# Performance work log

Measured on AMD Instinct MI355X. Metric: run time of the kernel, lower is better.

Reference implementation:

```python
import jax, jax.numpy as jnp
import numpy as np


def setup_inputs() -> dict:
    key = jax.random.key(0)
    k1, k2 = jax.random.split(key)
    out = jax.random.uniform(k1, (32, 128, 128, 9, 5), dtype=jnp.float32)
    target = jax.random.uniform(k2, (32, 128, 128, 3, 6), dtype=jnp.float32)
    return {"out": out, "target": target}


def _loss(out, target):
    # out: [B, GX, GY, A, 5], target: [B, GX, GY, Q, 6]
    B, GX, GY, Q, _ = target.shape
    A = out.shape[3]
    # the original loop breaks after qub == 0, so only the first gt per cell is used
    st = target[:, :, :, 0, :]            # [B, GX, GY, 6]
    pos = st[..., 5] > 0.8                # [B, GX, GY] positive-cell mask

    dtype = out.dtype
    # grid-cell centers zxdwx / zxdwy
    zx = (jnp.arange(GX, dtype=dtype) / GX + 1.0 / (2 * GX))[None, :, None, None]
    zy = (jnp.arange(GY, dtype=dtype) / GY + 1.0 / (2 * GY))[None, None, :, None]

    # gt box (center format) -> corners; broadcast over anchor dim
    acx = st[..., 0][..., None]
    acy = st[..., 1][..., None]
    aw = st[..., 2][..., None]
    ah = st[..., 3][..., None]
    ax1, ay1, ax2, ay2 = acx - aw / 2, acy - ah / 2, acx + aw / 2, acy + ah / 2

    # predicted box: offsets decoded relative to grid cell
    bcx = out[..., 0] - 0.5 + zx
    bcy = out[..., 1] - 0.5 + zy
    bw = out[..., 2] - 0.5 + 1.0 / GX
    bh = out[..., 3] - 0.5 + 1.0 / GY
    bx1, by1, bx2, by2 = bcx - bw / 2, bcy - bh / 2, bcx + bw / 2, bcy + bh / 2

    # IoU (intersection zeroed when either overlap extent <= 0)
    iw = jnp.minimum(ax2, bx2) - jnp.maximum(ax1, bx1)
    ih = jnp.minimum(ay2, by2) - jnp.maximum(ay1, by1)
    cross = jnp.where((iw > 0) & (ih > 0), iw * ih, 0.0)
    area_a = (ax2 - ax1) * (ay2 - ay1)
    area_b = (bx2 - bx1) * (by2 - by1)
    union = area_a + area_b - cross
    iou = cross / (union + 1e-6)

    # DIoU term: center distance over bound-box diagonal
    d = jnp.sqrt(((bx1 + bx2) / 2 - (ax1 + ax2) / 2) ** 2
                 + ((by1 + by2) / 2 - (ay1 + ay2) / 2) ** 2)
    cx1 = jnp.minimum(ax1, bx1)
    cy1 = jnp.minimum(ay1, by1)
    cx2 = jnp.maximum(ax2, bx2)
    cy2 = jnp.maximum(ay2, by2)
    c = jnp.sqrt((cx2 - cx1) ** 2 + (cy2 - cy1) ** 2)
    diou = iou - d ** 2 / c ** 2

    # CIoU aspect-ratio term
    v = (4.0 / np.pi ** 2) * (jnp.arctan((ax2 - ax1) / (ay2 - ay1))
                              - jnp.arctan((bx2 - bx1) / (by2 - by1))) ** 2
    alpha = v / (1 - iou + v)
    los = 1 - (diou - alpha * v)      # [B, GX, GY, A]

    obj = out[..., 4]
    posA = pos[..., None]             # broadcast mask over anchors

    jsq = (jnp.sum(pos) * A).astype(dtype)
    qit = (jnp.sum(~pos) * A).astype(dtype)
    allloss = jnp.sum(jnp.where(posA, los + (1 - obj), 0.0))
    jbb = jnp.sum(jnp.where(posA, iou, 0.0))
    huhuh = jnp.sum(jnp.where(posA, 1 - obj, 0.0))
    zsd = jnp.sum(jnp.where(posA, (1 - obj) ** 2, obj ** 2))

    return (allloss / jsq + zsd / (jsq + qit), jbb / jsq, huhuh / jsq)


def reference(out, target):
    return _loss(out, target)
```

## Files before the change

### kernel.cpp

```cpp
#include <hip/hip_runtime.h>
#include <math.h>

constexpr int kGX     = 128;
constexpr int kGY     = 128;
constexpr int kA      = 9;
constexpr int kNCells = 32 * kGX * kGY;
constexpr int kN      = kNCells * kA;

constexpr int kCellsPerWave = 32;
constexpr int kTiles        = kNCells / kCellsPerWave;
constexpr int kBlocks       = 4096;
constexpr int kWavesTotal   = kBlocks * 4;
static_assert(kWavesTotal == kTiles, "one tile per wave");

constexpr int kOutF4 = kCellsPerWave * 45 / 4;
constexpr int kTgtF4 = kCellsPerWave * 18 / 4;
constexpr int kTileF4 = kOutF4 + kTgtF4;

__device__ inline void gload_lds16(const void* gptr, void* lptr) {
    __builtin_amdgcn_global_load_lds(
        (const __attribute__((address_space(1))) unsigned int*)gptr,
        (__attribute__((address_space(3))) unsigned int*)lptr, 16, 0, 0);
}

__device__ inline float frcp(float x) { return __builtin_amdgcn_rcpf(x); }

__device__ inline float fast_atan(float r) {
    const float x = fabsf(r);
    const bool inv = x > 1.f;
    const float t = inv ? frcp(x) : x;
    const float t2 = t * t;
    float p = fmaf(t2, 0.0208351f, -0.0851330f);
    p = fmaf(t2, p, 0.1801410f);
    p = fmaf(t2, p, -0.3302995f);
    p = fmaf(t2, p, 0.9998660f);
    p = t * p;
    float res = inv ? (1.5707963f - p) : p;
    return r < 0.f ? -res : res;
}

__global__ __launch_bounds__(256)
void loss_main(const float* __restrict__ outp, const float* __restrict__ tgt,
               double* __restrict__ acc, int mode) {
    __shared__ float4 s_tile[4 * kTileF4];
    __shared__ double smem[4][5];

    const int lane = threadIdx.x & 63;
    const int wv   = threadIdx.x >> 6;
    float4* sw = s_tile + wv * kTileF4;
    const float* swf = (const float*)sw;
    const int tile = blockIdx.x * 4 + wv;

    {
        const float4* g = (const float4*)outp + (size_t)tile * kOutF4;
        #pragma unroll
        for (int j = 0; j < 5; ++j) gload_lds16(&g[j * 64 + lane], &sw[j * 64 + lane]);
        if (lane < kOutF4 - 320) gload_lds16(&g[320 + lane], &sw[320 + lane]);
        const float4* h = (const float4*)tgt + (size_t)tile * kTgtF4;
        #pragma unroll
        for (int j = 0; j < 2; ++j)
            gload_lds16(&h[j * 64 + lane], &sw[kOutF4 + j * 64 + lane]);
        if (lane < kTgtF4 - 128) gload_lds16(&h[128 + lane], &sw[kOutF4 + 128 + lane]);
    }
    __builtin_amdgcn_s_waitcnt(0);

    const int c = lane >> 1;
    const int s = lane & 1;
    const int cell = tile * kCellsPerWave + c;
    const int gy = cell & (kGY - 1);
    const int gx = (cell >> 7) & (kGX - 1);

    const float* st = swf + kOutF4 * 4 + c * 18;
    const float acx = st[0], acy = st[1], aw = st[2], ah = st[3], conf = st[5];
    const bool pos = conf > 0.8f;

    const float zx = (float)gx * (1.f / kGX) + 0.5f / kGX;
    const float zy = (float)gy * (1.f / kGY) + 0.5f / kGY;
    const float ax1 = acx - 0.5f * aw, ax2 = acx + 0.5f * aw;
    const float ay1 = acy - 0.5f * ah, ay2 = acy + 0.5f * ah;
    const float area_a = aw * ah;
    const float atan_a = fast_atan(aw * frcp(ah));

    const float* ob = swf + c * 45 + s * 5;

    float t_all = 0.f, t_jbb = 0.f, t_huh = 0.f, t_zsd = 0.f;
    float t_jsq = pos ? (s ? 4.f : 5.f) : 0.f;

    #pragma unroll
    for (int k = 0; k < 5; ++k) {
        const int a = s + 2 * k;
        const bool act = (a < kA);
        const float o0 = ob[k * 10 + 0], o1 = ob[k * 10 + 1], o2 = ob[k * 10 + 2];
        const float o3 = ob[k * 10 + 3], obj = ob[k * 10 + 4];

        const float bcx = o0 - 0.5f + zx;
        const float bcy = o1 - 0.5f + zy;
        const float bw  = o2 - 0.5f + (1.f / kGX);
        const float bh  = o3 - 0.5f + (1.f / kGY);
        const float bx1 = bcx - 0.5f * bw, bx2 = bcx + 0.5f * bw;
        const float by1 = bcy - 0.5f * bh, by2 = bcy + 0.5f * bh;

        const float iw = fminf(ax2, bx2) - fmaxf(ax1, bx1);
        const float ih = fminf(ay2, by2) - fmaxf(ay1, by1);
        const float cross = (iw > 0.f && ih > 0.f) ? iw * ih : 0.f;
        const float uni = area_a + bw * bh - cross;
        const float iou = cross * frcp(uni + 1e-6f);

        const float dx = bcx - acx, dy = bcy - acy;
        const float d2 = dx * dx + dy * dy;
        const float cw  = fmaxf(ax2, bx2) - fminf(ax1, bx1);
        const float chh = fmaxf(ay2, by2) - fminf(ay1, by1);
        const float c2 = cw * cw + chh * chh;
        const float diou = iou - d2 * frcp(c2);

        const float dat = atan_a - fast_atan(bw * frcp(bh));
        const float v = 0.4052847345693511f * dat * dat;
        const float alpha = v * frcp(1.f - iou + v);
        const float los = 1.f - (diou - alpha * v);
        const float om = 1.f - obj;

        const bool p = pos && act;
        t_all += p ? (los + om) : 0.f;
        t_jbb += p ? iou : 0.f;
        t_huh += p ? om : 0.f;
        t_zsd += p ? om * om : (act ? obj * obj : 0.f);
    }

    double vals[5] = {(double)t_jsq, (double)t_all, (double)t_jbb,
                      (double)t_huh, (double)t_zsd};
    #pragma unroll
    for (int i = 0; i < 5; ++i) {
        double x = vals[i];
        #pragma unroll
        for (int off = 32; off > 0; off >>= 1) x += __shfl_down(x, off, 64);
        vals[i] = x;
    }
    if (lane == 0) {
        #pragma unroll
        for (int i = 0; i < 5; ++i) smem[wv][i] = vals[i];
    }
    __syncthreads();
    if (threadIdx.x < 5) {
        const double sv = smem[0][threadIdx.x] + smem[1][threadIdx.x] +
                          smem[2][threadIdx.x] + smem[3][threadIdx.x];
        if (mode) acc[(size_t)blockIdx.x * 5 + threadIdx.x] = sv;
        else atomicAdd(&acc[threadIdx.x], sv);
    }
}

__global__ __launch_bounds__(256)
void loss_final(const double* __restrict__ acc, float* __restrict__ res, int n_part) {
    if (n_part > 0) {
        double v[5] = {0, 0, 0, 0, 0};
        for (int j = threadIdx.x; j < n_part; j += 256) {
            #pragma unroll
            for (int i = 0; i < 5; ++i) v[i] += acc[(size_t)j * 5 + i];
        }
        #pragma unroll
        for (int i = 0; i < 5; ++i) {
            double x = v[i];
            #pragma unroll
            for (int off = 32; off > 0; off >>= 1) x += __shfl_down(x, off, 64);
            v[i] = x;
        }
        __shared__ double sm[4][5];
        const int lane = threadIdx.x & 63, wv = threadIdx.x >> 6;
        if (lane == 0) {
            #pragma unroll
            for (int i = 0; i < 5; ++i) sm[wv][i] = v[i];
        }
        __syncthreads();
        if (threadIdx.x == 0) {
            #pragma unroll
            for (int i = 0; i < 5; ++i) v[i] = sm[0][i] + sm[1][i] + sm[2][i] + sm[3][i];
            const double jsq = v[0], total = (double)kN;
            res[0] = (float)(v[1] / jsq + v[4] / total);
            res[1] = (float)(v[2] / jsq);
            res[2] = (float)(v[3] / jsq);
        }
    } else if (threadIdx.x == 0) {
        const double jsq = acc[0], total = (double)kN;
        res[0] = (float)(acc[1] / jsq + acc[4] / total);
        res[1] = (float)(acc[2] / jsq);
        res[2] = (float)(acc[3] / jsq);
    }
}

extern "C" void kernel_launch(void* const* d_in, const int* in_sizes, int n_in,
                              void* d_out, int out_size, void* d_ws, size_t ws_size,
                              hipStream_t stream) {
    const float* outp = (const float*)d_in[0];
    const float* tgt  = (const float*)d_in[1];
    float* res = (float*)d_out;
    double* acc = (double*)d_ws;

    const bool partials = ws_size >= (size_t)kBlocks * 5 * sizeof(double);
    if (!partials) hipMemsetAsync(acc, 0, 5 * sizeof(double), stream);
    loss_main<<<kBlocks, 256, 0, stream>>>(outp, tgt, acc, partials ? 1 : 0);
    loss_final<<<1, 256, 0, stream>>>(acc, res, partials ? kBlocks : 0);
}
```

Baseline: 171.9 us.

## Process four tiles per wave with register-prefetched global loads

Each wave now handles four consecutive 32-cell tiles instead of one, with a quarter as many blocks. Global loads go into registers and are written to LDS, and the next tile's loads are issued before computing the current tile. The goal is to hide memory latency within a wave and spread the per-block reduction and atomic cost over more work. In exchange it uses more registers and leaves fewer waves in flight. The LDS reuse across iterations relies on per-wave ordering with no explicit barrier.

```diff
diff --git a/kernel.cpp b/kernel.cpp
--- a/kernel.cpp
+++ b/kernel.cpp
@@ -7,21 +7,15 @@
 constexpr int kNCells = 32 * kGX * kGY;
 constexpr int kN      = kNCells * kA;
 
-constexpr int kCellsPerWave = 32;
-constexpr int kTiles        = kNCells / kCellsPerWave;
-constexpr int kBlocks       = 4096;
-constexpr int kWavesTotal   = kBlocks * 4;
-static_assert(kWavesTotal == kTiles, "one tile per wave");
-
-constexpr int kOutF4 = kCellsPerWave * 45 / 4;
-constexpr int kTgtF4 = kCellsPerWave * 18 / 4;
+constexpr int kCellsPerTile = 32;
+constexpr int kTiles  = kNCells / kCellsPerTile;
+constexpr int kT      = 4;
+constexpr int kBlocks = kTiles / (4 * kT);
+static_assert(kBlocks * 4 * kT == kTiles, "exact cover");
+
+constexpr int kOutF4  = kCellsPerTile * 45 / 4;
+constexpr int kTgtF4  = kCellsPerTile * 18 / 4;
 constexpr int kTileF4 = kOutF4 + kTgtF4;
-
-__device__ inline void gload_lds16(const void* gptr, void* lptr) {
-    __builtin_amdgcn_global_load_lds(
-        (const __attribute__((address_space(1))) unsigned int*)gptr,
-        (__attribute__((address_space(3))) unsigned int*)lptr, 16, 0, 0);
-}
 
 __device__ inline float frcp(float x) { return __builtin_amdgcn_rcpf(x); }
 
@@ -49,81 +43,102 @@
     const int wv   = threadIdx.x >> 6;
     float4* sw = s_tile + wv * kTileF4;
     const float* swf = (const float*)sw;
-    const int tile = blockIdx.x * 4 + wv;
+    const int tile0 = (blockIdx.x * 4 + wv) * kT;
+
+    float4 orr[6], trr[3];
 
     {
-        const float4* g = (const float4*)outp + (size_t)tile * kOutF4;
-        #pragma unroll
-        for (int j = 0; j < 5; ++j) gload_lds16(&g[j * 64 + lane], &sw[j * 64 + lane]);
-        if (lane < kOutF4 - 320) gload_lds16(&g[320 + lane], &sw[320 + lane]);
-        const float4* h = (const float4*)tgt + (size_t)tile * kTgtF4;
-        #pragma unroll
-        for (int j = 0; j < 2; ++j)
-            gload_lds16(&h[j * 64 + lane], &sw[kOutF4 + j * 64 + lane]);
-        if (lane < kTgtF4 - 128) gload_lds16(&h[128 + lane], &sw[kOutF4 + 128 + lane]);
-    }
-    __builtin_amdgcn_s_waitcnt(0);
-
-    const int c = lane >> 1;
-    const int s = lane & 1;
-    const int cell = tile * kCellsPerWave + c;
-    const int gy = cell & (kGY - 1);
-    const int gx = (cell >> 7) & (kGX - 1);
-
-    const float* st = swf + kOutF4 * 4 + c * 18;
-    const float acx = st[0], acy = st[1], aw = st[2], ah = st[3], conf = st[5];
-    const bool pos = conf > 0.8f;
-
-    const float zx = (float)gx * (1.f / kGX) + 0.5f / kGX;
-    const float zy = (float)gy * (1.f / kGY) + 0.5f / kGY;
-    const float ax1 = acx - 0.5f * aw, ax2 = acx + 0.5f * aw;
-    const float ay1 = acy - 0.5f * ah, ay2 = acy + 0.5f * ah;
-    const float area_a = aw * ah;
-    const float atan_a = fast_atan(aw * frcp(ah));
-
-    const float* ob = swf + c * 45 + s * 5;
-
-    float t_all = 0.f, t_jbb = 0.f, t_huh = 0.f, t_zsd = 0.f;
-    float t_jsq = pos ? (s ? 4.f : 5.f) : 0.f;
-
-    #pragma unroll
-    for (int k = 0; k < 5; ++k) {
-        const int a = s + 2 * k;
-        const bool act = (a < kA);
-        const float o0 = ob[k * 10 + 0], o1 = ob[k * 10 + 1], o2 = ob[k * 10 + 2];
-        const float o3 = ob[k * 10 + 3], obj = ob[k * 10 + 4];
-
-        const float bcx = o0 - 0.5f + zx;
-        const float bcy = o1 - 0.5f + zy;
-        const float bw  = o2 - 0.5f + (1.f / kGX);
-        const float bh  = o3 - 0.5f + (1.f / kGY);
-        const float bx1 = bcx - 0.5f * bw, bx2 = bcx + 0.5f * bw;
-        const float by1 = bcy - 0.5f * bh, by2 = bcy + 0.5f * bh;
-
-        const float iw = fminf(ax2, bx2) - fmaxf(ax1, bx1);
-        const float ih = fminf(ay2, by2) - fmaxf(ay1, by1);
-        const float cross = (iw > 0.f && ih > 0.f) ? iw * ih : 0.f;
-        const float uni = area_a + bw * bh - cross;
-        const float iou = cross * frcp(uni + 1e-6f);
-
-        const float dx = bcx - acx, dy = bcy - acy;
-        const float d2 = dx * dx + dy * dy;
-        const float cw  = fmaxf(ax2, bx2) - fminf(ax1, bx1);
-        const float chh = fmaxf(ay2, by2) - fminf(ay1, by1);
-        const float c2 = cw * cw + chh * chh;
-        const float diou = iou - d2 * frcp(c2);
-
-        const float dat = atan_a - fast_atan(bw * frcp(bh));
-        const float v = 0.4052847345693511f * dat * dat;
-        const float alpha = v * frcp(1.f - iou + v);
-        const float los = 1.f - (diou - alpha * v);
-        const float om = 1.f - obj;
-
-        const bool p = pos && act;
-        t_all += p ? (los + om) : 0.f;
-        t_jbb += p ? iou : 0.f;
-        t_huh += p ? om : 0.f;
-        t_zsd += p ? om * om : (act ? obj * obj : 0.f);
+        const float4* g = (const float4*)outp + (size_t)tile0 * kOutF4;
+        #pragma unroll
+        for (int j = 0; j < 5; ++j) orr[j] = g[j * 64 + lane];
+        if (lane < 40) orr[5] = g[320 + lane];
+        const float4* h = (const float4*)tgt + (size_t)tile0 * kTgtF4;
+        trr[0] = h[lane]; trr[1] = h[64 + lane];
+        if (lane < 16) trr[2] = h[128 + lane];
+    }
+
+    const int c  = lane >> 1;
+    const int sa = lane & 1;
+    float t_jsq = 0.f, t_all = 0.f, t_jbb = 0.f, t_huh = 0.f, t_zsd = 0.f;
+
+    for (int t = 0; t < kT; ++t) {
+        #pragma unroll
+        for (int j = 0; j < 5; ++j) sw[j * 64 + lane] = orr[j];
+        if (lane < 40) sw[320 + lane] = orr[5];
+        sw[360 + lane] = trr[0]; sw[424 + lane] = trr[1];
+        if (lane < 16) sw[488 + lane] = trr[2];
+        __builtin_amdgcn_s_waitcnt(0xC07F);
+
+        if (t + 1 < kT) {
+            const int tn = tile0 + t + 1;
+            const float4* g = (const float4*)outp + (size_t)tn * kOutF4;
+            #pragma unroll
+            for (int j = 0; j < 5; ++j) orr[j] = g[j * 64 + lane];
+            if (lane < 40) orr[5] = g[320 + lane];
+            const float4* h = (const float4*)tgt + (size_t)tn * kTgtF4;
+            trr[0] = h[lane]; trr[1] = h[64 + lane];
+            if (lane < 16) trr[2] = h[128 + lane];
+        }
+
+        const int tile = tile0 + t;
+        const int cell = tile * kCellsPerTile + c;
+        const int gy = cell & (kGY - 1);
+        const int gx = (cell >> 7) & (kGX - 1);
+
+        const float* st = swf + 4 * kOutF4 + c * 18;
+        const float acx = st[0], acy = st[1], aw = st[2], ah = st[3], conf = st[5];
+        const bool pos = conf > 0.8f;
+
+        const float zx = (float)gx * (1.f / kGX) + 0.5f / kGX;
+        const float zy = (float)gy * (1.f / kGY) + 0.5f / kGY;
+        const float ax1 = acx - 0.5f * aw, ax2 = acx + 0.5f * aw;
+        const float ay1 = acy - 0.5f * ah, ay2 = acy + 0.5f * ah;
+        const float area_a = aw * ah;
+        const float atan_a = fast_atan(aw * frcp(ah));
+
+        const float* ob = swf + c * 45 + sa * 5;
+
+        t_jsq += pos ? (sa ? 4.f : 5.f) : 0.f;
+
+        #pragma unroll
+        for (int k = 0; k < 5; ++k) {
+            const int a = sa + 2 * k;
+            const bool act = (a < kA);
+            const float o0 = ob[k * 10 + 0], o1 = ob[k * 10 + 1], o2 = ob[k * 10 + 2];
+            const float o3 = ob[k * 10 + 3], obj = ob[k * 10 + 4];
+
+            const float bcx = o0 - 0.5f + zx;
+            const float bcy = o1 - 0.5f + zy;
+            const float bw  = o2 - 0.5f + (1.f / kGX);
+            const float bh  = o3 - 0.5f + (1.f / kGY);
+            const float bx1 = bcx - 0.5f * bw, bx2 = bcx + 0.5f * bw;
+            const float by1 = bcy - 0.5f * bh, by2 = bcy + 0.5f * bh;
+
+            const float iw = fminf(ax2, bx2) - fmaxf(ax1, bx1);
+            const float ih = fminf(ay2, by2) - fmaxf(ay1, by1);
+            const float cross = (iw > 0.f && ih > 0.f) ? iw * ih : 0.f;
+            const float uni = area_a + bw * bh - cross;
+            const float iou = cross * frcp(uni + 1e-6f);
+
+            const float dx = bcx - acx, dy = bcy - acy;
+            const float d2 = dx * dx + dy * dy;
+            const float cw  = fmaxf(ax2, bx2) - fminf(ax1, bx1);
+            const float chh = fmaxf(ay2, by2) - fminf(ay1, by1);
+            const float c2 = cw * cw + chh * chh;
+            const float diou = iou - d2 * frcp(c2);
+
+            const float dat = atan_a - fast_atan(bw * frcp(bh));
+            const float v = 0.4052847345693511f * dat * dat;
+            const float alpha = v * frcp(1.f - iou + v);
+            const float los = 1.f - (diou - alpha * v);
+            const float om = 1.f - obj;
+
+            const bool p = pos && act;
+            t_all += p ? (los + om) : 0.f;
+            t_jbb += p ? iou : 0.f;
+            t_huh += p ? om : 0.f;
+            t_zsd += p ? om * om : (act ? obj * obj : 0.f);
+        }
     }
 
     double vals[5] = {(double)t_jsq, (double)t_all, (double)t_jbb,
```

Result: slower. 202.9 us (+18.1%).

## Halve cells per wave, use four lanes per cell, reduce in float

Applied to the files above, without the earlier changes.

Each wave now takes 16 cells instead of 32, so the grid doubles to 8192 blocks and each lane evaluates at most 3 anchors instead of 5. Launch bounds now request 8 blocks per CU. The in-wave shuffle reduction moves from double to float, with the per-block sum still done in double. The aim is more parallelism and shorter per-thread dependency chains at the cost of more blocks, a larger partials array for the final kernel, and slightly lower float precision in the wave reduction.

```diff
diff --git a/kernel.cpp b/kernel.cpp
--- a/kernel.cpp
+++ b/kernel.cpp
@@ -7,14 +7,13 @@
 constexpr int kNCells = 32 * kGX * kGY;
 constexpr int kN      = kNCells * kA;
 
-constexpr int kCellsPerWave = 32;
-constexpr int kTiles        = kNCells / kCellsPerWave;
-constexpr int kBlocks       = 4096;
-constexpr int kWavesTotal   = kBlocks * 4;
-static_assert(kWavesTotal == kTiles, "one tile per wave");
+constexpr int kCellsPerTile = 16;
+constexpr int kTiles  = kNCells / kCellsPerTile;
+constexpr int kBlocks = kTiles / 4;
+static_assert(kBlocks * 4 == kTiles, "exact cover");
 
-constexpr int kOutF4 = kCellsPerWave * 45 / 4;
-constexpr int kTgtF4 = kCellsPerWave * 18 / 4;
+constexpr int kOutF4  = kCellsPerTile * 45 / 4;
+constexpr int kTgtF4  = kCellsPerTile * 18 / 4;
 constexpr int kTileF4 = kOutF4 + kTgtF4;
 
 __device__ inline void gload_lds16(const void* gptr, void* lptr) {
@@ -39,11 +38,11 @@
     return r < 0.f ? -res : res;
 }
 
-__global__ __launch_bounds__(256)
+__global__ __launch_bounds__(256, 8)
 void loss_main(const float* __restrict__ outp, const float* __restrict__ tgt,
                double* __restrict__ acc, int mode) {
     __shared__ float4 s_tile[4 * kTileF4];
-    __shared__ double smem[4][5];
+    __shared__ float smem[4][5];
 
     const int lane = threadIdx.x & 63;
     const int wv   = threadIdx.x >> 6;
@@ -53,24 +52,22 @@
 
     {
         const float4* g = (const float4*)outp + (size_t)tile * kOutF4;
-        #pragma unroll
-        for (int j = 0; j < 5; ++j) gload_lds16(&g[j * 64 + lane], &sw[j * 64 + lane]);
-        if (lane < kOutF4 - 320) gload_lds16(&g[320 + lane], &sw[320 + lane]);
+        gload_lds16(&g[lane], &sw[lane]);
+        gload_lds16(&g[64 + lane], &sw[64 + lane]);
+        if (lane < kOutF4 - 128) gload_lds16(&g[128 + lane], &sw[128 + lane]);
         const float4* h = (const float4*)tgt + (size_t)tile * kTgtF4;
-        #pragma unroll
-        for (int j = 0; j < 2; ++j)
-            gload_lds16(&h[j * 64 + lane], &sw[kOutF4 + j * 64 + lane]);
-        if (lane < kTgtF4 - 128) gload_lds16(&h[128 + lane], &sw[kOutF4 + 128 + lane]);
+        gload_lds16(&h[lane], &sw[kOutF4 + lane]);
+        if (lane < kTgtF4 - 64) gload_lds16(&h[64 + lane], &sw[kOutF4 + 64 + lane]);
     }
     __builtin_amdgcn_s_waitcnt(0);
 
-    const int c = lane >> 1;
-    const int s = lane & 1;
-    const int cell = tile * kCellsPerWave + c;
+    const int c = lane >> 2;
+    const int p = lane & 3;
+    const int cell = tile * kCellsPerTile + c;
     const int gy = cell & (kGY - 1);
     const int gx = (cell >> 7) & (kGX - 1);
 
-    const float* st = swf + kOutF4 * 4 + c * 18;
+    const float* st = swf + 4 * kOutF4 + c * 18;
     const float acx = st[0], acy = st[1], aw = st[2], ah = st[3], conf = st[5];
     const bool pos = conf > 0.8f;
 
@@ -81,17 +78,18 @@
     const float area_a = aw * ah;
     const float atan_a = fast_atan(aw * frcp(ah));
 
-    const float* ob = swf + c * 45 + s * 5;
+    const float* ob = swf + c * 45 + p * 5;
 
     float t_all = 0.f, t_jbb = 0.f, t_huh = 0.f, t_zsd = 0.f;
-    float t_jsq = pos ? (s ? 4.f : 5.f) : 0.f;
+    float t_jsq = pos ? (p == 0 ? 3.f : 2.f) : 0.f;
 
     #pragma unroll
-    for (int k = 0; k < 5; ++k) {
-        const int a = s + 2 * k;
+    for (int k = 0; k < 3; ++k) {
+        const int a = p + 4 * k;
         const bool act = (a < kA);
-        const float o0 = ob[k * 10 + 0], o1 = ob[k * 10 + 1], o2 = ob[k * 10 + 2];
-        const float o3 = ob[k * 10 + 3], obj = ob[k * 10 + 4];
+        const int off = act ? k * 20 : 0;
+        const float o0 = ob[off + 0], o1 = ob[off + 1], o2 = ob[off + 2];
+        const float o3 = ob[off + 3], obj = ob[off + 4];
 
         const float bcx = o0 - 0.5f + zx;
         const float bcy = o1 - 0.5f + zy;
@@ -119,18 +117,17 @@
         const float los = 1.f - (diou - alpha * v);
         const float om = 1.f - obj;
 
-        const bool p = pos && act;
-        t_all += p ? (los + om) : 0.f;
-        t_jbb += p ? iou : 0.f;
-        t_huh += p ? om : 0.f;
-        t_zsd += p ? om * om : (act ? obj * obj : 0.f);
+        const bool pp = pos && act;
+        t_all += pp ? (los + om) : 0.f;
+        t_jbb += pp ? iou : 0.f;
+        t_huh += pp ? om : 0.f;
+        t_zsd += pp ? om * om : (act ? obj * obj : 0.f);
     }
 
-    double vals[5] = {(double)t_jsq, (double)t_all, (double)t_jbb,
-                      (double)t_huh, (double)t_zsd};
+    float vals[5] = {t_jsq, t_all, t_jbb, t_huh, t_zsd};
     #pragma unroll
     for (int i = 0; i < 5; ++i) {
-        double x = vals[i];
+        float x = vals[i];
         #pragma unroll
         for (int off = 32; off > 0; off >>= 1) x += __shfl_down(x, off, 64);
         vals[i] = x;
@@ -141,8 +138,8 @@
     }
     __syncthreads();
     if (threadIdx.x < 5) {
-        const double sv = smem[0][threadIdx.x] + smem[1][threadIdx.x] +
-                          smem[2][threadIdx.x] + smem[3][threadIdx.x];
+        const double sv = (double)smem[0][threadIdx.x] + (double)smem[1][threadIdx.x] +
+                          (double)smem[2][threadIdx.x] + (double)smem[3][threadIdx.x];
         if (mode) acc[(size_t)blockIdx.x * 5 + threadIdx.x] = sv;
         else atomicAdd(&acc[threadIdx.x], sv);
     }
```

New measurement: 175.9 us. 1.02x slower.
